# Kernel optimization log

Measured on AMD Instinct MI355X. Metric: run time of the kernel, lower is better.

## Reference

```python
import jax, jax.numpy as jnp
import numpy as np


def _topk_axis(x, k, axis, largest):
    # lax.top_k works on the last axis, largest, sorted descending.
    xm = jnp.moveaxis(x, axis, -1)
    if largest:
        vals, idx = jax.lax.top_k(xm, k)
    else:
        vals, idx = jax.lax.top_k(-xm, k)
        vals = -vals  # ascending smallest-k, matching torch.topk(largest=False, sorted=True)
    return jnp.moveaxis(vals, -1, axis), jnp.moveaxis(idx, -1, axis)


def setup_inputs() -> dict:
    key = jax.random.key(0)
    k0, k1, k2 = jax.random.split(key, 3)
    v_0 = jax.random.normal(k0, (4096, 32000), dtype=jnp.float32)
    v_1 = jax.random.normal(k1, (8, 16, 64, 4096), dtype=jnp.float32)
    v_2 = jax.random.normal(k2, (100000, 512), dtype=jnp.float32)
    return {"v_0": v_0, "v_1": v_1, "v_2": v_2}


def reference(v_0, v_1, v_2):
    # TopK_0: k=2, dim=1, largest, sorted
    v_4, v_5 = _topk_axis(v_0, 2, 1, largest=True)
    # TopK_1: k=4, dim=3, smallest, sorted
    v_7, v_8 = _topk_axis(v_1, 4, 3, largest=False)
    # TopK_2: k=3, dim=0, largest, sorted
    v_10, v_11 = _topk_axis(v_2, 3, 0, largest=True)
    return (v_4, v_5, v_7, v_8, v_10, v_11)
```

## Files before the change

### kernel.cpp

```cpp
#include <hip/hip_runtime.h>
#include <limits.h>
#include <math.h>

typedef unsigned long long u64;
typedef unsigned int u32;
typedef float f32x4 __attribute__((ext_vector_type(4)));
typedef float f32x2 __attribute__((ext_vector_type(2)));

__device__ __forceinline__ u32 f2ord(float v) {
    u32 u = __float_as_uint(v);
    return u ^ (((u32)((int)u >> 31)) | 0x80000000u);
}
__device__ __forceinline__ float ord2f(u32 s) {
    u32 u = (s & 0x80000000u) ? (s & 0x7FFFFFFFu) : ~s;
    return __uint_as_float(u);
}
__device__ __forceinline__ u64 keylg(float v, u32 i) { return ((u64)f2ord(v) << 32) | (u64)(~i); }
__device__ __forceinline__ u64 keysm(float v, u32 i) { return ((u64)f2ord(v) << 32) | (u64)i; }
__device__ __forceinline__ float val_of(u64 k) { return ord2f((u32)(k >> 32)); }
__device__ __forceinline__ float idxf_lg(u64 k) { return (float)(~(u32)k); }
__device__ __forceinline__ float idxf_sm(u64 k) { return (float)((u32)k); }

__device__ __forceinline__ u64 mx64(u64 a, u64 b) { return a > b ? a : b; }
__device__ __forceinline__ u64 mn64(u64 a, u64 b) { return a < b ? a : b; }

__device__ __forceinline__ void ins3_lg(u64& s0, u64& s1, u64& s2, u64 k) {
    u64 t0 = mx64(s0, k), r0 = mn64(s0, k);
    u64 t1 = mx64(s1, r0), r1 = mn64(s1, r0);
    s0 = t0; s1 = t1; s2 = mx64(s2, r1);
}

__device__ __forceinline__ void ce_max(u64& a, u64& b) { u64 h = mx64(a, b), l = mn64(a, b); a = h; b = l; }
__device__ __forceinline__ void ce_min(u64& a, u64& b) { u64 l = mn64(a, b), h = mx64(a, b); a = l; b = h; }

__device__ __forceinline__ void merge2_lg(u64& a0, u64& a1, u64 b0, u64 b1) {
    u64 l0 = mx64(a0, b1), l1 = mx64(a1, b0);
    a0 = mx64(l0, l1); a1 = mn64(l0, l1);
}
__device__ __forceinline__ void merge3_lg(u64& a0, u64& a1, u64& a2, u64 b0, u64 b1, u64 b2) {
    u64 l0 = mx64(a0, b2), l1 = mx64(a1, b1), l2 = mx64(a2, b0);
    ce_max(l0, l1); ce_max(l1, l2); ce_max(l0, l1);
    a0 = l0; a1 = l1; a2 = l2;
}
__device__ __forceinline__ void merge4_sm(u64& a0, u64& a1, u64& a2, u64& a3,
                                          u64 b0, u64 b1, u64 b2, u64 b3) {
    u64 l0 = mn64(a0, b3), l1 = mn64(a1, b2), l2 = mn64(a2, b1), l3 = mn64(a3, b0);
    ce_min(l0, l2); ce_min(l1, l3); ce_min(l0, l1); ce_min(l2, l3);
    a0 = l0; a1 = l1; a2 = l2; a3 = l3;
}

__device__ __forceinline__ u64 shx64(u64 v, int m) {
    u32 hi = __shfl_xor((u32)(v >> 32), m);
    u32 lo = __shfl_xor((u32)v, m);
    return ((u64)hi << 32) | (u64)lo;
}

__device__ __forceinline__ void top2of4_lg(f32x4 f, u32 b, u64& o0, u64& o1) {
    u64 k0 = keylg(f.x, b), k1 = keylg(f.y, b + 1);
    u64 k2 = keylg(f.z, b + 2), k3 = keylg(f.w, b + 3);
    u64 h0 = mx64(k0, k1), l0 = mn64(k0, k1);
    u64 h1 = mx64(k2, k3), l1 = mn64(k2, k3);
    u64 m0 = mx64(h0, l1), m1 = mx64(l0, h1);
    o0 = mx64(m0, m1); o1 = mn64(m0, m1);
}

__device__ __forceinline__ void sort4_sm(f32x4 f, u32 bse,
                                         u64& b0, u64& b1, u64& b2, u64& b3) {
    u64 k0 = keysm(f.x, bse), k1 = keysm(f.y, bse + 1);
    u64 k2 = keysm(f.z, bse + 2), k3 = keysm(f.w, bse + 3);
    u64 p0 = mn64(k0, k1), p1 = mx64(k0, k1);
    u64 q0 = mn64(k2, k3), q1 = mx64(k2, k3);
    b0 = mn64(p0, q0); u64 t = mx64(p0, q0);
    b3 = mx64(p1, q1); u64 u = mn64(p1, q1);
    b1 = mn64(t, u); b2 = mx64(t, u);
}

#define NTL4(p) __builtin_nontemporal_load((const f32x4*)(p))
#define NTL2(p) __builtin_nontemporal_load((const f32x2*)(p))

__global__ __launch_bounds__(256) void mega_kernel(
    const float* __restrict__ x0, float* __restrict__ o0v, float* __restrict__ o0i,
    const float* __restrict__ x1, float* __restrict__ o1v, float* __restrict__ o1i,
    const float* __restrict__ x2, u64* __restrict__ part, int rpb, int do_p1)
{
    const int bid  = blockIdx.x;
    const int wave = threadIdx.x >> 6;
    const int lane = threadIdx.x & 63;

    if (bid < 1024) {
        const int row = bid * 4 + wave;
        const f32x4* xr = (const f32x4*)(x0 + (size_t)row * 32000);
        u64 sA0 = 0, sA1 = 0, sB0 = 0, sB1 = 0;

        int v = lane;
        for (int it = 0; it < 15; ++it, v += 512) {
            f32x4 t0 = NTL4(&xr[v]);
            f32x4 t1 = NTL4(&xr[v + 64]);
            f32x4 t2 = NTL4(&xr[v + 128]);
            f32x4 t3 = NTL4(&xr[v + 192]);
            f32x4 t4 = NTL4(&xr[v + 256]);
            f32x4 t5 = NTL4(&xr[v + 320]);
            f32x4 t6 = NTL4(&xr[v + 384]);
            f32x4 t7 = NTL4(&xr[v + 448]);
            u64 w0, w1;
            top2of4_lg(t0, (u32)(v * 4),         w0, w1); merge2_lg(sA0, sA1, w0, w1);
            top2of4_lg(t1, (u32)((v + 64) * 4),  w0, w1); merge2_lg(sB0, sB1, w0, w1);
            top2of4_lg(t2, (u32)((v + 128) * 4), w0, w1); merge2_lg(sA0, sA1, w0, w1);
            top2of4_lg(t3, (u32)((v + 192) * 4), w0, w1); merge2_lg(sB0, sB1, w0, w1);
            top2of4_lg(t4, (u32)((v + 256) * 4), w0, w1); merge2_lg(sA0, sA1, w0, w1);
            top2of4_lg(t5, (u32)((v + 320) * 4), w0, w1); merge2_lg(sB0, sB1, w0, w1);
            top2of4_lg(t6, (u32)((v + 384) * 4), w0, w1); merge2_lg(sA0, sA1, w0, w1);
            top2of4_lg(t7, (u32)((v + 448) * 4), w0, w1); merge2_lg(sB0, sB1, w0, w1);
        }
        {
            f32x4 t0 = NTL4(&xr[v]);
            f32x4 t1 = NTL4(&xr[v + 64]);
            f32x4 t2 = NTL4(&xr[v + 128]);
            f32x4 t3 = NTL4(&xr[v + 192]);
            f32x4 t4 = NTL4(&xr[v + 256]);
            u64 w0, w1;
            top2of4_lg(t0, (u32)(v * 4),         w0, w1); merge2_lg(sA0, sA1, w0, w1);
            top2of4_lg(t1, (u32)((v + 64) * 4),  w0, w1); merge2_lg(sB0, sB1, w0, w1);
            top2of4_lg(t2, (u32)((v + 128) * 4), w0, w1); merge2_lg(sA0, sA1, w0, w1);
            top2of4_lg(t3, (u32)((v + 192) * 4), w0, w1); merge2_lg(sB0, sB1, w0, w1);
            top2of4_lg(t4, (u32)((v + 256) * 4), w0, w1); merge2_lg(sA0, sA1, w0, w1);
        }
        merge2_lg(sA0, sA1, sB0, sB1);

        for (int m = 1; m < 64; m <<= 1) {
            u64 b0 = shx64(sA0, m), b1 = shx64(sA1, m);
            merge2_lg(sA0, sA1, b0, b1);
        }
        if (lane == 0) {
            o0v[row * 2 + 0] = val_of(sA0);  o0v[row * 2 + 1] = val_of(sA1);
            o0i[row * 2 + 0] = idxf_lg(sA0); o0i[row * 2 + 1] = idxf_lg(sA1);
        }

    } else if (bid < 1536) {
        if (!do_p1) return;
        const int blk = bid - 1024;
        const int c0  = threadIdx.x * 2;
        int rbeg = blk * rpb;
        int rend = rbeg + rpb; if (rend > 100000) rend = 100000;

        u64 a0 = 0, a1 = 0, a2 = 0;
        u64 b0 = 0, b1 = 0, b2 = 0;

#define P1LOAD(r) NTL2(x2 + (size_t)(r) * 512 + c0)
#define P1UPD(f, rr) \
        ins3_lg(a0, a1, a2, keylg((f).x, (u32)(rr))); \
        ins3_lg(b0, b1, b2, keylg((f).y, (u32)(rr)))

        int r = rbeg;
        for (; r + 7 < rend; r += 8) {
            f32x2 f0 = P1LOAD(r);
            f32x2 f1 = P1LOAD(r + 1);
            f32x2 f2 = P1LOAD(r + 2);
            f32x2 f3 = P1LOAD(r + 3);
            f32x2 f4 = P1LOAD(r + 4);
            f32x2 f5 = P1LOAD(r + 5);
            f32x2 f6 = P1LOAD(r + 6);
            f32x2 f7 = P1LOAD(r + 7);
            P1UPD(f0, r);     P1UPD(f1, r + 1); P1UPD(f2, r + 2); P1UPD(f3, r + 3);
            P1UPD(f4, r + 4); P1UPD(f5, r + 5); P1UPD(f6, r + 6); P1UPD(f7, r + 7);
        }
        for (; r < rend; ++r) {
            f32x2 f0 = P1LOAD(r);
            P1UPD(f0, r);
        }
#undef P1LOAD
#undef P1UPD

        u64* base = part + (size_t)blk * 1536;
        base[0 * 512 + c0] = a0; base[0 * 512 + c0 + 1] = b0;
        base[1 * 512 + c0] = a1; base[1 * 512 + c0 + 1] = b1;
        base[2 * 512 + c0] = a2; base[2 * 512 + c0 + 1] = b2;

    } else {
        const int row = (bid - 1536) * 4 + wave;
        const f32x4* xr = (const f32x4*)(x1 + (size_t)row * 4096);
        u64 s0 = ~0ull, s1 = ~0ull, s2 = ~0ull, s3 = ~0ull;

#define K1UPD(f, b) { u64 c0_, c1_, c2_, c3_;                      \
        sort4_sm((f), (u32)(b), c0_, c1_, c2_, c3_);               \
        merge4_sm(s0, s1, s2, s3, c0_, c1_, c2_, c3_); }

        int v = lane;
        for (int it = 0; it < 2; ++it, v += 512) {
            f32x4 t0 = NTL4(&xr[v]);
            f32x4 t1 = NTL4(&xr[v + 64]);
            f32x4 t2 = NTL4(&xr[v + 128]);
            f32x4 t3 = NTL4(&xr[v + 192]);
            f32x4 t4 = NTL4(&xr[v + 256]);
            f32x4 t5 = NTL4(&xr[v + 320]);
            f32x4 t6 = NTL4(&xr[v + 384]);
            f32x4 t7 = NTL4(&xr[v + 448]);
            K1UPD(t0, v * 4);
            K1UPD(t1, (v + 64) * 4);
            K1UPD(t2, (v + 128) * 4);
            K1UPD(t3, (v + 192) * 4);
            K1UPD(t4, (v + 256) * 4);
            K1UPD(t5, (v + 320) * 4);
            K1UPD(t6, (v + 384) * 4);
            K1UPD(t7, (v + 448) * 4);
        }
#undef K1UPD

        for (int m = 1; m < 64; m <<= 1) {
            u64 b0 = shx64(s0, m), b1 = shx64(s1, m);
            u64 b2 = shx64(s2, m), b3 = shx64(s3, m);
            merge4_sm(s0, s1, s2, s3, b0, b1, b2, b3);
        }
        if (lane == 0) {
            o1v[row * 4 + 0] = val_of(s0);  o1v[row * 4 + 1] = val_of(s1);
            o1v[row * 4 + 2] = val_of(s2);  o1v[row * 4 + 3] = val_of(s3);
            o1i[row * 4 + 0] = idxf_sm(s0); o1i[row * 4 + 1] = idxf_sm(s1);
            o1i[row * 4 + 2] = idxf_sm(s2); o1i[row * 4 + 3] = idxf_sm(s3);
        }
    }
}

__global__ __launch_bounds__(256) void topk2_reduce(
    const u64* __restrict__ part, float* __restrict__ outv, float* __restrict__ outi)
{
    const int wave = threadIdx.x >> 6;
    const int lane = threadIdx.x & 63;
    const int col  = blockIdx.x * 4 + wave;

    u64 a0 = 0, a1 = 0, a2 = 0;
#pragma unroll
    for (int j = 0; j < 8; ++j) {
        const u64* q = part + (size_t)(lane + 64 * j) * 1536 + col;
        merge3_lg(a0, a1, a2, q[0], q[512], q[1024]);
    }
    for (int m = 1; m < 64; m <<= 1) {
        u64 b0 = shx64(a0, m), b1 = shx64(a1, m), b2 = shx64(a2, m);
        merge3_lg(a0, a1, a2, b0, b1, b2);
    }

    if (lane == 0) {
        outv[0 * 512 + col] = val_of(a0);
        outv[1 * 512 + col] = val_of(a1);
        outv[2 * 512 + col] = val_of(a2);
        outi[0 * 512 + col] = idxf_lg(a0);
        outi[1 * 512 + col] = idxf_lg(a1);
        outi[2 * 512 + col] = idxf_lg(a2);
    }
}

__global__ __launch_bounds__(256) void topk2_direct(
    const float* __restrict__ x, float* __restrict__ outv, float* __restrict__ outi)
{
    const int col = blockIdx.x * 256 + threadIdx.x;
    u64 a0 = 0, a1 = 0, a2 = 0;
    for (int r = 0; r < 100000; ++r) {
        float v = x[(size_t)r * 512 + col];
        ins3_lg(a0, a1, a2, keylg(v, (u32)r));
    }
    outv[0 * 512 + col] = val_of(a0);
    outv[1 * 512 + col] = val_of(a1);
    outv[2 * 512 + col] = val_of(a2);
    outi[0 * 512 + col] = idxf_lg(a0);
    outi[1 * 512 + col] = idxf_lg(a1);
    outi[2 * 512 + col] = idxf_lg(a2);
}

extern "C" void kernel_launch(void* const* d_in, const int* in_sizes, int n_in,
                              void* d_out, int out_size, void* d_ws, size_t ws_size,
                              hipStream_t stream) {
    const float* v0 = (const float*)d_in[0];
    const float* v1 = (const float*)d_in[1];
    const float* v2 = (const float*)d_in[2];
    float* out = (float*)d_out;

    float* o_v4  = out;
    float* o_v5  = out + 8192;
    float* o_v7  = out + 16384;
    float* o_v8  = out + 49152;
    float* o_v10 = out + 81920;
    float* o_v11 = out + 83456;

    const int NB = 512;
    int rpb = (100000 + NB - 1) / NB;
    size_t need = (size_t)NB * 3 * 512 * sizeof(u64);

    if (ws_size >= need) {
        u64* part = (u64*)d_ws;
        mega_kernel<<<3584, 256, 0, stream>>>(v0, o_v4, o_v5,
                                              v1, o_v7, o_v8,
                                              v2, part, rpb, 1);
        topk2_reduce<<<128, 256, 0, stream>>>(part, o_v10, o_v11);
    } else {
        mega_kernel<<<3584, 256, 0, stream>>>(v0, o_v4, o_v5,
                                              v1, o_v7, o_v8,
                                              v2, (u64*)d_ws, rpb, 0);
        topk2_direct<<<2, 256, 0, stream>>>(v2, o_v10, o_v11);
    }
}
```

Measured before the change: 154.6 us.

## Fuse column top-k reduction into mega kernel via atomic completion counter

Removes the separate topk2_reduce launch and appends 128 extra blocks to the mega kernel. Each phase-1 producer block signals completion by atomically incrementing a global counter, and the new blocks spin until all 512 partials are present before reducing them. This saves a kernel launch and its tail gap, but adds a hipMemsetAsync per call. It also relies on the spinning blocks being scheduled after the producers; they come last in block order, so the wait should normally be short, though this is not guaranteed.

```diff
diff --git a/kernel.cpp b/kernel.cpp
--- a/kernel.cpp
+++ b/kernel.cpp
@@ -81,7 +81,8 @@
 __global__ __launch_bounds__(256) void mega_kernel(
     const float* __restrict__ x0, float* __restrict__ o0v, float* __restrict__ o0i,
     const float* __restrict__ x1, float* __restrict__ o1v, float* __restrict__ o1i,
-    const float* __restrict__ x2, u64* __restrict__ part, int rpb, int do_p1)
+    const float* __restrict__ x2, u64* __restrict__ part, u32* __restrict__ counter,
+    float* __restrict__ o2v, float* __restrict__ o2i, int rpb, int do_p1)
 {
     const int bid  = blockIdx.x;
     const int wave = threadIdx.x >> 6;
@@ -176,7 +177,11 @@
         base[1 * 512 + c0] = a1; base[1 * 512 + c0 + 1] = b1;
         base[2 * 512 + c0] = a2; base[2 * 512 + c0 + 1] = b2;
 
-    } else {
+        __threadfence();
+        __syncthreads();
+        if (threadIdx.x == 0) atomicAdd(counter, 1u);
+
+    } else if (bid < 3584) {
         const int row = (bid - 1536) * 4 + wave;
         const f32x4* xr = (const f32x4*)(x1 + (size_t)row * 4096);
         u64 s0 = ~0ull, s1 = ~0ull, s2 = ~0ull, s3 = ~0ull;
@@ -217,34 +222,36 @@
             o1i[row * 4 + 0] = idxf_sm(s0); o1i[row * 4 + 1] = idxf_sm(s1);
             o1i[row * 4 + 2] = idxf_sm(s2); o1i[row * 4 + 3] = idxf_sm(s3);
         }
-    }
-}
-
-__global__ __launch_bounds__(256) void topk2_reduce(
-    const u64* __restrict__ part, float* __restrict__ outv, float* __restrict__ outi)
-{
-    const int wave = threadIdx.x >> 6;
-    const int lane = threadIdx.x & 63;
-    const int col  = blockIdx.x * 4 + wave;
-
-    u64 a0 = 0, a1 = 0, a2 = 0;
+
+    } else {
+        if (!do_p1) return;
+        if (threadIdx.x == 0) {
+            while (__hip_atomic_load(counter, __ATOMIC_ACQUIRE,
+                                     __HIP_MEMORY_SCOPE_AGENT) < 512u) {
+                __builtin_amdgcn_s_sleep(2);
+            }
+        }
+        __syncthreads();
+
+        const int col = (bid - 3584) * 4 + wave;
+        u64 a0 = 0, a1 = 0, a2 = 0;
 #pragma unroll
-    for (int j = 0; j < 8; ++j) {
-        const u64* q = part + (size_t)(lane + 64 * j) * 1536 + col;
-        merge3_lg(a0, a1, a2, q[0], q[512], q[1024]);
-    }
-    for (int m = 1; m < 64; m <<= 1) {
-        u64 b0 = shx64(a0, m), b1 = shx64(a1, m), b2 = shx64(a2, m);
-        merge3_lg(a0, a1, a2, b0, b1, b2);
-    }
-
-    if (lane == 0) {
-        outv[0 * 512 + col] = val_of(a0);
-        outv[1 * 512 + col] = val_of(a1);
-        outv[2 * 512 + col] = val_of(a2);
-        outi[0 * 512 + col] = idxf_lg(a0);
-        outi[1 * 512 + col] = idxf_lg(a1);
-        outi[2 * 512 + col] = idxf_lg(a2);
+        for (int j = 0; j < 8; ++j) {
+            const u64* q = part + (size_t)(lane + 64 * j) * 1536 + col;
+            merge3_lg(a0, a1, a2, q[0], q[512], q[1024]);
+        }
+        for (int m = 1; m < 64; m <<= 1) {
+            u64 b0 = shx64(a0, m), b1 = shx64(a1, m), b2 = shx64(a2, m);
+            merge3_lg(a0, a1, a2, b0, b1, b2);
+        }
+        if (lane == 0) {
+            o2v[0 * 512 + col] = val_of(a0);
+            o2v[1 * 512 + col] = val_of(a1);
+            o2v[2 * 512 + col] = val_of(a2);
+            o2i[0 * 512 + col] = idxf_lg(a0);
+            o2i[1 * 512 + col] = idxf_lg(a1);
+            o2i[2 * 512 + col] = idxf_lg(a2);
+        }
     }
 }
 
@@ -282,18 +289,22 @@
 
     const int NB = 512;
     int rpb = (100000 + NB - 1) / NB;
-    size_t need = (size_t)NB * 3 * 512 * sizeof(u64);
+    size_t part_bytes = (size_t)NB * 3 * 512 * sizeof(u64);
+    size_t need = part_bytes + 64;
 
     if (ws_size >= need) {
-        u64* part = (u64*)d_ws;
-        mega_kernel<<<3584, 256, 0, stream>>>(v0, o_v4, o_v5,
+        u64* part    = (u64*)d_ws;
+        u32* counter = (u32*)((char*)d_ws + part_bytes);
+        hipMemsetAsync(counter, 0, sizeof(u32), stream);
+        mega_kernel<<<3712, 256, 0, stream>>>(v0, o_v4, o_v5,
                                               v1, o_v7, o_v8,
-                                              v2, part, rpb, 1);
-        topk2_reduce<<<128, 256, 0, stream>>>(part, o_v10, o_v11);
+                                              v2, part, counter,
+                                              o_v10, o_v11, rpb, 1);
     } else {
         mega_kernel<<<3584, 256, 0, stream>>>(v0, o_v4, o_v5,
                                               v1, o_v7, o_v8,
-                                              v2, (u64*)d_ws, rpb, 0);
+                                              v2, (u64*)d_ws, (u32*)d_ws,
+                                              o_v10, o_v11, rpb, 0);
         topk2_direct<<<2, 256, 0, stream>>>(v2, o_v10, o_v11);
     }
 }
```

Result: slower. 264.5 us (+71.0%).
